# Kernel optimization log

Measured on AMD Instinct MI355X. Metric: run time of the kernel, lower is better.

The kernel has to match this reference:

```python
import jax, jax.numpy as jnp
import numpy as np

BETA = 1.0
B, S, D = 4, 4096, 1024


def setup_inputs() -> dict:
    key = jax.random.key(0)
    k_x, k_q, k_k, k_v = jax.random.split(key, 4)
    scale = 1.0 / np.sqrt(D)  # nn.Linear-like init scale
    x = jax.random.normal(k_x, (B, S, D), dtype=jnp.float32)
    Wq = jax.random.uniform(k_q, (D, D), dtype=jnp.float32, minval=-scale, maxval=scale)
    Wk = jax.random.uniform(k_k, (D, D), dtype=jnp.float32, minval=-scale, maxval=scale)
    Wv = jax.random.uniform(k_v, (D, D), dtype=jnp.float32, minval=-scale, maxval=scale)
    return {"x": x, "Wq": Wq, "Wk": Wk, "Wv": Wv}


def reference(x, Wq, Wk, Wv):
    # nn.Linear(bias=False): y = x @ W.T
    q = jnp.einsum('bsd,ed->bse', x, Wq)
    k = jnp.einsum('bsd,ed->bse', x, Wk)
    v = jnp.einsum('bsd,ed->bse', x, Wv)
    scores = jnp.einsum('bqd,bkd->bqk', q, k)          # [B, S, S]
    attn = jax.nn.softmax(BETA * scores, axis=-1)
    attended = jnp.einsum('bqk,bkd->bqd', attn, v)
    y = attended + x
    return y / jnp.linalg.norm(y, axis=-1, keepdims=True)
```

## Files before the change

### kernel.cpp

```cpp
#include <hip/hip_runtime.h>

typedef unsigned short u16;
typedef _Float16 half8 __attribute__((ext_vector_type(8)));
typedef __attribute__((ext_vector_type(4))) float f32x4;

constexpr int NB = 4;
constexpr int S  = 4096;
constexpr int D  = 1024;

__device__ __forceinline__ u16 h2u(_Float16 h) {
    union { _Float16 h; u16 u; } v; v.h = h; return v.u;
}

__device__ __forceinline__ void async16(const void* g, void* l) {
    __builtin_amdgcn_global_load_lds(
        (const __attribute__((address_space(1))) unsigned int*)g,
        (__attribute__((address_space(3))) unsigned int*)l, 16, 0, 0);
}

#define BAR()  __builtin_amdgcn_s_barrier()
#define SFEN() __builtin_amdgcn_sched_barrier(0)

#define MF(AF, BF, QM, QN)                                                     \
  do {                                                                         \
    _Pragma("unroll") for (int m_ = 0; m_ < 4; ++m_)                           \
    _Pragma("unroll") for (int n_ = 0; n_ < 2; ++n_)                           \
    _Pragma("unroll") for (int k_ = 0; k_ < 2; ++k_)                           \
      acc[(QM)*4 + m_][(QN)*2 + n_] = __builtin_amdgcn_mfma_f32_16x16x32_f16(  \
          AF[m_][k_], BF[n_][k_], acc[(QM)*4 + m_][(QN)*2 + n_], 0, 0, 0);     \
  } while (0)

#define RDA(dst, bp0, bp1, qm)                                                 \
  _Pragma("unroll") for (int m_ = 0; m_ < 4; ++m_) {                           \
    dst[m_][0] = *(const half8*)(bp0 + (qm) * 4096 + m_ * 1024);               \
    dst[m_][1] = *(const half8*)(bp1 + (qm) * 4096 + m_ * 1024); }
#define RDB(dst, bp0, bp1, qn)                                                 \
  _Pragma("unroll") for (int n_ = 0; n_ < 2; ++n_) {                           \
    dst[n_][0] = *(const half8*)(bp0 + (qn) * 2048 + n_ * 1024);               \
    dst[n_][1] = *(const half8*)(bp1 + (qn) * 2048 + n_ * 1024); }

#define HALF(RAd, RBd, OAd, OBd, rA0, rA1, rB0, rB1, KO, KN)                   \
  {                                              \
    RDA(a0, rA0, rA1, 0)                                                       \
    RDB(b0, rB0, rB1, 0)                                                       \
    issue(Am, OAd, rsA + 64, KO);                                              \
    __builtin_amdgcn_s_setprio(1); MF(a0, b0, 0, 0);                           \
    __builtin_amdgcn_s_setprio(0);                                             \
    RDB(b1, rB0, rB1, 1)                                                       \
    BAR(); SFEN();                                                             \
                                                      \
    issue(Bm, OBd, rsB + 32, KO);                                              \
    __builtin_amdgcn_s_setprio(1); MF(a0, b1, 0, 1);                           \
    __builtin_amdgcn_s_setprio(0);                                             \
    RDA(a1, rA0, rA1, 1)                                                       \
    BAR(); SFEN();                                                             \
                                                      \
    issue(Am, RAd, rsA, KN);                                                   \
    __builtin_amdgcn_s_setprio(1); MF(a1, b0, 1, 0);                           \
    __builtin_amdgcn_s_setprio(0);                                             \
    BAR(); SFEN();                                                             \
                                                      \
    issue(Bm, RBd, rsB, KN);                                                   \
    __builtin_amdgcn_s_setprio(1); MF(a1, b1, 1, 1);                           \
    __builtin_amdgcn_s_setprio(0);                                             \
    asm volatile("s_waitcnt vmcnt(4)" ::: "memory");                           \
    BAR(); SFEN();                                                             \
  }

__device__ __forceinline__ void gemm256(
    const u16* __restrict__ Am, const u16* __restrict__ Bm, const int K,
    u16* lds, f32x4 acc[8][4])
{
    const int tid  = threadIdx.x;
    const int lane = tid & 63;
    const int w    = tid >> 6;
    const int wm   = w >> 2;
    const int wn   = w & 3;
    const int quad = lane >> 4;
    const int lrow = lane & 15;
    const int s7   = lrow & 7;
    const int rl   = lane >> 3;
    const int gc8  = ((lane & 7) ^ rl) * 8;
    const int rsA  = (wm << 7) + ((w & 3) << 4);
    const int rsB  = ((w >> 1) << 6) + ((w & 1) << 4);

    u16* const As0 = lds;
    u16* const Bs0 = lds + 16384;
    u16* const As1 = lds + 32768;
    u16* const Bs1 = lds + 49152;

    const int lt0 = lrow * 64 + ((quad ^ s7) * 8);
    const int lt1 = lrow * 64 + (((4 + quad) ^ s7) * 8);
    const u16* const bA00 = As0 + wm * 8192 + lt0;
    const u16* const bA01 = As0 + wm * 8192 + lt1;
    const u16* const bA10 = As1 + wm * 8192 + lt0;
    const u16* const bA11 = As1 + wm * 8192 + lt1;
    const u16* const bB00 = Bs0 + wn * 4096 + lt0;
    const u16* const bB01 = Bs0 + wn * 4096 + lt1;
    const u16* const bB10 = Bs1 + wn * 4096 + lt0;
    const u16* const bB11 = Bs1 + wn * 4096 + lt1;

    auto issue = [&](const u16* M, u16* dst, int rs, int k0) {
        async16(M + (size_t)(rs + rl) * K + k0 + gc8,
                dst + (size_t)(rs)     * 64 + (size_t)lane * 8);
        async16(M + (size_t)(rs + 8 + rl) * K + k0 + gc8,
                dst + (size_t)(rs + 8) * 64 + (size_t)lane * 8);
    };

    issue(Am, As0, rsA,      0);
    issue(Bm, Bs0, rsB,      0);
    issue(Am, As0, rsA + 64, 0);
    issue(Bm, Bs0, rsB + 32, 0);
    issue(Am, As1, rsA,      64);
    issue(Bm, Bs1, rsB,      64);
    asm volatile("s_waitcnt vmcnt(4)" ::: "memory");
    BAR(); SFEN();

    half8 a0[4][2], a1[4][2], b0[2][2], b1[2][2];
    const int km = K - 1;
    const int NI = K >> 7;
    for (int it = 0; it < NI; ++it) {
        const int kb  = it << 7;
        const int t1k = (kb + 64)  & km;
        const int t2k = (kb + 128) & km;
        const int t3k = (kb + 192) & km;
        HALF(As0, Bs0, As1, Bs1, bA00, bA01, bB00, bB01, t1k, t2k)
        HALF(As1, Bs1, As0, Bs0, bA10, bA11, bB10, bB11, t2k, t3k)
    }
}

__global__ __launch_bounds__(256) void cvt_kernel(
    const float* __restrict__ in, u16* __restrict__ out, int n8)
{
    const int i = blockIdx.x * 256 + threadIdx.x;
    if (i >= n8) return;
    const float4 a = *(const float4*)(in + (size_t)i * 8);
    const float4 b = *(const float4*)(in + (size_t)i * 8 + 4);
    half8 h;
    h[0] = (_Float16)a.x; h[1] = (_Float16)a.y;
    h[2] = (_Float16)a.z; h[3] = (_Float16)a.w;
    h[4] = (_Float16)b.x; h[5] = (_Float16)b.y;
    h[6] = (_Float16)b.z; h[7] = (_Float16)b.w;
    *(half8*)(out + (size_t)i * 8) = h;
}

__global__ __launch_bounds__(512, 2) void qkv_kernel(
    const u16* __restrict__ x16, const u16* __restrict__ W16,
    u16* __restrict__ Q, u16* __restrict__ Kb, u16* __restrict__ V)
{
    __shared__ __align__(16) u16 lds[65536];
    const int lin = blockIdx.x + (blockIdx.y << 6) + (blockIdx.z << 8);
    const int swz = (lin & 7) * 96 + (lin >> 3);
    const int bx = swz & 63, by = (swz >> 6) & 3, bz = swz >> 8;

    const int tile_m = bx * 256;
    const int tile_n = by * 256;
    const u16* W = W16 + (size_t)bz * D * D;
    u16* out = (bz == 0) ? Q : (bz == 1) ? Kb : V;

    f32x4 acc[8][4];
#pragma unroll
    for (int i = 0; i < 8; ++i)
#pragma unroll
        for (int j = 0; j < 4; ++j) acc[i][j] = (f32x4)0.0f;

    gemm256(x16 + (size_t)tile_m * D, W + (size_t)tile_n * D, D, lds, acc);

    const int tid = threadIdx.x, lane = tid & 63, w = tid >> 6;
    const int quad = lane >> 4, lrow = lane & 15;
    const int wm = w >> 2, wn = w & 3;
#pragma unroll
    for (int mi = 0; mi < 8; ++mi)
#pragma unroll
        for (int r = 0; r < 4; ++r) {
            const int row = tile_m + wm * 128 + mi * 16 + quad * 4 + r;
#pragma unroll
            for (int ni = 0; ni < 4; ++ni) {
                const int col = tile_n + wn * 64 + ni * 16 + lrow;
                out[(size_t)row * D + col] = h2u((_Float16)acc[mi][ni][r]);
            }
        }
}

__global__ __launch_bounds__(256) void transpose_v(
    const u16* __restrict__ V, u16* __restrict__ Vt)
{
    __shared__ u16 t[64][72];
    const int sg = blockIdx.x * 64;
    const int b  = sg >> 12;
    const int s0 = sg & (S - 1);
    const int e0 = blockIdx.y * 64;
    const int tid = threadIdx.x;
#pragma unroll
    for (int p = 0; p < 2; ++p) {
        const int v  = tid + 256 * p;
        const int sr = v >> 3, sc = (v & 7) * 8;
        half8 vec = *(const half8*)(V + (size_t)(sg + sr) * D + e0 + sc);
        *(half8*)&t[sr][sc] = vec;
    }
    __syncthreads();
#pragma unroll
    for (int p = 0; p < 2; ++p) {
        const int v  = tid + 256 * p;
        const int e  = v >> 3, s8 = (v & 7) * 8;
        u16 o[8];
#pragma unroll
        for (int j = 0; j < 8; ++j) o[j] = t[s8 + j][e];
        *(uint4*)(Vt + (size_t)b * D * S + (size_t)(e0 + e) * S + s0 + s8) = *(const uint4*)o;
    }
}

__global__ __launch_bounds__(512, 2) void scores_kernel(
    const u16* __restrict__ Q, const u16* __restrict__ Kb, u16* __restrict__ P)
{
    __shared__ __align__(16) u16 lds[65536];
    const int lin = blockIdx.x + ((blockIdx.y + (blockIdx.z << 4)) << 4);
    const int swz = ((lin & 7) << 7) + (lin >> 3);
    const int bx = swz & 15, by = (swz >> 4) & 15, bz = swz >> 8;

    const int b = bz;
    const int tile_m = bx * 256;
    const int tile_n = by * 256;
    const u16* Ab = Q  + (size_t)b * S * D + (size_t)tile_m * D;
    const u16* Bv = Kb + (size_t)b * S * D + (size_t)tile_n * D;

    f32x4 acc[8][4];
#pragma unroll
    for (int i = 0; i < 8; ++i)
#pragma unroll
        for (int j = 0; j < 4; ++j) acc[i][j] = (f32x4)0.0f;

    gemm256(Ab, Bv, D, lds, acc);

    u16* Pb = P + (size_t)b * S * S;
    const int tid = threadIdx.x, lane = tid & 63, w = tid >> 6;
    const int quad = lane >> 4, lrow = lane & 15;
    const int wm = w >> 2, wn = w & 3;
#pragma unroll
    for (int mi = 0; mi < 8; ++mi)
#pragma unroll
        for (int r = 0; r < 4; ++r) {
            const int row = tile_m + wm * 128 + mi * 16 + quad * 4 + r;
#pragma unroll
            for (int ni = 0; ni < 4; ++ni) {
                const int col = tile_n + wn * 64 + ni * 16 + lrow;
                Pb[(size_t)row * S + col] = h2u((_Float16)acc[mi][ni][r]);
            }
        }
}

__global__ __launch_bounds__(256) void softmax_kernel(u16* __restrict__ P)
{
    const size_t row = blockIdx.x;
    u16* p = P + row * S;
    const int tid = threadIdx.x;

    half8 h0 = *(const half8*)(p + tid * 16);
    half8 h1 = *(const half8*)(p + tid * 16 + 8);
    float v[16];
#pragma unroll
    for (int i = 0; i < 8; ++i) { v[i] = (float)h0[i]; v[8 + i] = (float)h1[i]; }

    float m = v[0];
#pragma unroll
    for (int i = 1; i < 16; ++i) m = fmaxf(m, v[i]);
#pragma unroll
    for (int off = 32; off > 0; off >>= 1) m = fmaxf(m, __shfl_xor(m, off));

    __shared__ float redm[4], reds[4];
    const int wid = tid >> 6;
    if ((tid & 63) == 0) redm[wid] = m;
    __syncthreads();
    m = fmaxf(fmaxf(redm[0], redm[1]), fmaxf(redm[2], redm[3]));

    float e[16], s = 0.f;
#pragma unroll
    for (int i = 0; i < 16; ++i) { e[i] = __expf(v[i] - m); s += e[i]; }
#pragma unroll
    for (int off = 32; off > 0; off >>= 1) s += __shfl_xor(s, off);
    if ((tid & 63) == 0) reds[wid] = s;
    __syncthreads();
    s = reds[0] + reds[1] + reds[2] + reds[3];
    const float inv = 1.0f / s;

#pragma unroll
    for (int i = 0; i < 8; ++i) {
        h0[i] = (_Float16)(e[i] * inv);
        h1[i] = (_Float16)(e[8 + i] * inv);
    }
    *(half8*)(p + tid * 16)     = h0;
    *(half8*)(p + tid * 16 + 8) = h1;
}

__global__ __launch_bounds__(512, 2) void pv_kernel(
    const u16* __restrict__ P, const u16* __restrict__ Vt,
    const float* __restrict__ x, float* __restrict__ y)
{
    __shared__ __align__(16) u16 lds[65536];
    const int lin = blockIdx.x + (blockIdx.y << 4) + (blockIdx.z << 6);
    const int swz = ((lin & 7) << 5) + (lin >> 3);
    const int bx = swz & 15, by = (swz >> 4) & 3, bz = swz >> 6;

    const int b = bz;
    const int tile_m = bx * 256;
    const int tile_n = by * 256;
    const u16* Ab = P  + (size_t)b * S * S + (size_t)tile_m * S;
    const u16* Bv = Vt + (size_t)b * D * S + (size_t)tile_n * S;

    f32x4 acc[8][4];
#pragma unroll
    for (int i = 0; i < 8; ++i)
#pragma unroll
        for (int j = 0; j < 4; ++j) acc[i][j] = (f32x4)0.0f;

    gemm256(Ab, Bv, S, lds, acc);

    const int tid = threadIdx.x, lane = tid & 63, w = tid >> 6;
    const int quad = lane >> 4, lrow = lane & 15;
    const int wm = w >> 2, wn = w & 3;

#pragma unroll
    for (int mi = 0; mi < 8; ++mi)
#pragma unroll
        for (int r = 0; r < 4; ++r) {
            const int row = tile_m + wm * 128 + mi * 16 + quad * 4 + r;
            const size_t base = ((size_t)b * S + row) * D;
#pragma unroll
            for (int ni = 0; ni < 4; ++ni) {
                const int col = tile_n + wn * 64 + ni * 16 + lrow;
                y[base + col] = acc[mi][ni][r] + x[base + col];
            }
        }
}

__global__ __launch_bounds__(256) void normalize_kernel(float* __restrict__ y)
{
    const size_t row = blockIdx.x;
    const int tid = threadIdx.x;
    float4* p = (float4*)(y + row * D) + tid;

    float4 v = *p;
    float ss = v.x * v.x + v.y * v.y + v.z * v.z + v.w * v.w;
#pragma unroll
    for (int off = 32; off > 0; off >>= 1) ss += __shfl_xor(ss, off);

    __shared__ float red[4];
    const int wid = tid >> 6;
    if ((tid & 63) == 0) red[wid] = ss;
    __syncthreads();
    const float inv = rsqrtf(red[0] + red[1] + red[2] + red[3]);

    v.x *= inv; v.y *= inv; v.z *= inv; v.w *= inv;
    *p = v;
}

extern "C" void kernel_launch(void* const* d_in, const int* in_sizes, int n_in,
                              void* d_out, int out_size, void* d_ws, size_t ws_size,
                              hipStream_t stream) {
    const float* x  = (const float*)d_in[0];
    const float* Wq = (const float*)d_in[1];
    const float* Wk = (const float*)d_in[2];
    const float* Wv = (const float*)d_in[3];
    float* out = (float*)d_out;

    char* ws = (char*)d_ws;
    const size_t MB = 1ull << 20;
    u16* Q   = (u16*)(ws);
    u16* Kb  = (u16*)(ws + 32 * MB);
    u16* Vt  = (u16*)(ws + 64 * MB);
    u16* P   = (u16*)(ws + 96 * MB);
    u16* V   = P;
    u16* x16 = Vt;
    u16* W16 = (u16*)(ws + 218 * MB);

    dim3 blk(256);
    dim3 blk2(512);
    cvt_kernel <<<dim3(NB * S * D / 8 / 256), blk, 0, stream>>>(x,  x16, NB * S * D / 8);
    cvt_kernel <<<dim3(D * D / 8 / 256), blk, 0, stream>>>(Wq, W16,             D * D / 8);
    cvt_kernel <<<dim3(D * D / 8 / 256), blk, 0, stream>>>(Wk, W16 + (size_t)D * D, D * D / 8);
    cvt_kernel <<<dim3(D * D / 8 / 256), blk, 0, stream>>>(Wv, W16 + (size_t)2 * D * D, D * D / 8);

    qkv_kernel    <<<dim3(NB * S / 256, D / 256, 3), blk2, 0, stream>>>(x16, W16, Q, Kb, V);
    transpose_v   <<<dim3(NB * S / 64, D / 64), blk, 0, stream>>>(V, Vt);
    scores_kernel <<<dim3(S / 256, S / 256, NB), blk2, 0, stream>>>(Q, Kb, P);
    softmax_kernel<<<dim3(NB * S), blk, 0, stream>>>(P);
    pv_kernel     <<<dim3(S / 256, D / 256, NB), blk2, 0, stream>>>(P, Vt, x, out);
    normalize_kernel<<<dim3(NB * S), blk, 0, stream>>>(out);
}
```

Before: 549.7 us.

## Simplify GEMM pipeline to plain double buffering with one barrier per tile

```diff
diff --git a/kernel.cpp b/kernel.cpp
--- a/kernel.cpp
+++ b/kernel.cpp
@@ -39,31 +39,23 @@
     dst[n_][0] = *(const half8*)(bp0 + (qn) * 2048 + n_ * 1024);               \
     dst[n_][1] = *(const half8*)(bp1 + (qn) * 2048 + n_ * 1024); }
 
-#define HALF(RAd, RBd, OAd, OBd, rA0, rA1, rB0, rB1, KO, KN)                   \
-  {                                              \
+#define TILE(OAd, OBd, rA0, rA1, rB0, rB1, KN)                                 \
+  {                                                                            \
     RDA(a0, rA0, rA1, 0)                                                       \
     RDB(b0, rB0, rB1, 0)                                                       \
-    issue(Am, OAd, rsA + 64, KO);                                              \
-    __builtin_amdgcn_s_setprio(1); MF(a0, b0, 0, 0);                           \
+    issue(Am, OAd, rsA,      KN);                                              \
+    issue(Am, OAd, rsA + 64, KN);                                              \
+    issue(Bm, OBd, rsB,      KN);                                              \
+    issue(Bm, OBd, rsB + 32, KN);                                              \
+    __builtin_amdgcn_s_setprio(1);                                             \
+    MF(a0, b0, 0, 0);                                                          \
+    RDB(b1, rB0, rB1, 1)                                                       \
+    MF(a0, b1, 0, 1);                                                          \
+    RDA(a1, rA0, rA1, 1)                                                       \
+    MF(a1, b0, 1, 0);                                                          \
+    MF(a1, b1, 1, 1);                                                          \
     __builtin_amdgcn_s_setprio(0);                                             \
-    RDB(b1, rB0, rB1, 1)                                                       \
-    BAR(); SFEN();                                                             \
-                                                      \
-    issue(Bm, OBd, rsB + 32, KO);                                              \
-    __builtin_amdgcn_s_setprio(1); MF(a0, b1, 0, 1);                           \
-    __builtin_amdgcn_s_setprio(0);                                             \
-    RDA(a1, rA0, rA1, 1)                                                       \
-    BAR(); SFEN();                                                             \
-                                                      \
-    issue(Am, RAd, rsA, KN);                                                   \
-    __builtin_amdgcn_s_setprio(1); MF(a1, b0, 1, 0);                           \
-    __builtin_amdgcn_s_setprio(0);                                             \
-    BAR(); SFEN();                                                             \
-                                                      \
-    issue(Bm, RBd, rsB, KN);                                                   \
-    __builtin_amdgcn_s_setprio(1); MF(a1, b1, 1, 1);                           \
-    __builtin_amdgcn_s_setprio(0);                                             \
-    asm volatile("s_waitcnt vmcnt(4)" ::: "memory");                           \
+    asm volatile("s_waitcnt vmcnt(0)" ::: "memory");                           \
     BAR(); SFEN();                                                             \
   }
 
@@ -108,12 +100,10 @@
     };
 
     issue(Am, As0, rsA,      0);
+    issue(Am, As0, rsA + 64, 0);
     issue(Bm, Bs0, rsB,      0);
-    issue(Am, As0, rsA + 64, 0);
     issue(Bm, Bs0, rsB + 32, 0);
-    issue(Am, As1, rsA,      64);
-    issue(Bm, Bs1, rsB,      64);
-    asm volatile("s_waitcnt vmcnt(4)" ::: "memory");
+    asm volatile("s_waitcnt vmcnt(0)" ::: "memory");
     BAR(); SFEN();
 
     half8 a0[4][2], a1[4][2], b0[2][2], b1[2][2];
@@ -123,9 +113,8 @@
         const int kb  = it << 7;
         const int t1k = (kb + 64)  & km;
         const int t2k = (kb + 128) & km;
-        const int t3k = (kb + 192) & km;
-        HALF(As0, Bs0, As1, Bs1, bA00, bA01, bB00, bB01, t1k, t2k)
-        HALF(As1, Bs1, As0, Bs0, bA10, bA11, bB10, bB11, t2k, t3k)
+        TILE(As1, Bs1, bA00, bA01, bB00, bB01, t1k)
+        TILE(As0, Bs0, bA10, bA11, bB10, bB11, t2k)
     }
 }
 
```

Result: faster. 516.6 us (-6.0%).
